# Optimization experiments

Measured on AMD Instinct MI355X. Metric: run time of the kernel, lower is better.

## Reference

```python
import jax, jax.numpy as jnp
import numpy as np

T, B, A, I, H, L = 256, 64, 512, 1024, 1024, 2
STDV = 1.0 / np.sqrt(H)

def _uniform(key, shape):
    return jax.random.uniform(key, shape, jnp.float32, -STDV, STDV)

def setup_inputs() -> dict:
    key = jax.random.key(0)
    ks = jax.random.split(key, 11)
    return {
        "attention": jax.random.normal(ks[0], (T, B, A), jnp.float32),
        "x": jax.random.normal(ks[1], (T, B, I), jnp.float32),
        "ping": jax.random.normal(ks[2], (B,), jnp.float32),  # unused by module
        "h0": jax.random.normal(ks[3], (L, B, H), jnp.float32),
        "c0": jax.random.normal(ks[4], (L, B, H), jnp.float32),
        "weight_ah": _uniform(ks[5], (L, A, 4 * H)),
        "weight_ih": _uniform(ks[6], (L, I, 4 * H)),  # input_size == hidden_size so layers stack
        "weight_hh": _uniform(ks[7], (L, H, 4 * H)),
        "bias_ah": _uniform(ks[8], (L, 4 * H)),
        "bias_ih": _uniform(ks[9], (L, 4 * H)),
        "bias_hh": _uniform(ks[10], (L, 4 * H)),
    }

def reference(attention, x, ping, h0, c0, weight_ah, weight_ih, weight_hh, bias_ah, bias_ih, bias_hh):
    # Faithful to SACILSTM.forward: only attention[0] is used (fixed across t),
    # ping is unused; per layer l, state is initialized from init_states[l].
    a0 = attention[0]  # [B, A]
    inputs = x  # [T, B, I]
    h_lasts, c_lasts = [], []
    for l in range(h0.shape[0]):
        w_hh = weight_hh[l]
        # Precompute the time-invariant + input-dependent part of the gates.
        const = a0 @ weight_ah[l] + bias_ah[l] + bias_ih[l] + bias_hh[l]  # [B, 4H]
        xg = jnp.einsum('tbi,ij->tbj', inputs, weight_ih[l]) + const  # [T, B, 4H]

        def step(carry, xg_t):
            h, c = carry
            gates = xg_t + h @ w_hh
            i_g, f_g, g_g, o_g = jnp.split(gates, 4, axis=-1)
            c = jax.nn.sigmoid(f_g) * c + jax.nn.sigmoid(i_g) * jnp.tanh(g_g)
            h = jax.nn.sigmoid(o_g) * jnp.tanh(c)
            return (h, c), h

        (h_T, c_T), hs = jax.lax.scan(step, (h0[l], c0[l]), xg)
        inputs = hs  # [T, B, H] feeds next layer
        h_lasts.append(h_T)
        c_lasts.append(c_T)
    # (self.h[:, -1], (self.h[-1], self.c[-1])) flattened
    return hs, jnp.stack(h_lasts), jnp.stack(c_lasts)
```

## Files before the change

kernel.cpp:

```cpp
#include <hip/hip_runtime.h>
#include <hip/hip_bf16.h>
#include <stdint.h>

#define TT 256
#define BB 64
#define AA 512
#define II 1024
#define HH 1024
#define LL 2
#define BH 65536
#define B4H 262144
#define OUT_HL 16777216
#define OUT_CL (16777216 + 131072)
#define NBLK 256

typedef __attribute__((ext_vector_type(8))) short bf16x8;
typedef __attribute__((ext_vector_type(4))) float f32x4;
typedef __attribute__((ext_vector_type(4))) unsigned int u32x4;
typedef __attribute__((ext_vector_type(2))) unsigned int u32x2;

__device__ __forceinline__ ushort f2bf(float v) {
    union { float f; uint32_t u; } x; x.f = v;
    uint32_t r = x.u + 0x7fff + ((x.u >> 16) & 1);
    return (ushort)(r >> 16);
}

__device__ __forceinline__ float sigf(float x) {
    return 1.f / (1.f + __expf(-x));
}


__global__ __launch_bounds__(256) void k_prep_wt(const float* __restrict__ wih,
                                                 const float* __restrict__ whh,
                                                 ushort* __restrict__ Wt) {
    __shared__ ushort tile[64][65];
    const int l = blockIdx.z;
    const int k0 = blockIdx.x * 64;
    const int col0 = blockIdx.y * 64;
    const int tid = threadIdx.x;
    const int cl = tid & 63, ks = tid >> 6;
    const float* src;
    int krow0;
    if (k0 < 1024) { src = wih + (size_t)l * 1024 * 4096; krow0 = k0; }
    else           { src = whh + (size_t)l * 1024 * 4096; krow0 = k0 - 1024; }
#pragma unroll
    for (int i = 0; i < 16; ++i) {
        int kl = ks + i * 4;
        tile[kl][cl] = f2bf(src[(size_t)(krow0 + kl) * 4096 + col0 + cl]);
    }
    __syncthreads();
    const int g0 = col0 >> 10, ub = col0 & 1023;
    ushort* dst = Wt + (size_t)l * 4096 * 2048;
    const int klane = tid & 63;
#pragma unroll
    for (int i = 0; i < 16; ++i) {
        int cl2 = (tid >> 6) + i * 4;
        int row = (ub + cl2) * 4 + g0;
        ushort* p = dst + (size_t)row * 2048 + k0 + klane;
        uint v = (uint)tile[klane][cl2];
        asm volatile("global_store_short %0, %1, off sc0 sc1"
                     :: "v"(p), "v"(v) : "memory");
    }
}

__global__ __launch_bounds__(256) void k_cast_x(const float* __restrict__ x,
                                                ushort* __restrict__ xbfF) {
    int i = blockIdx.x * 256 + threadIdx.x;
    int k8 = i & 127, b = (i >> 7) & 63, t = i >> 13;
    const float4* xs = (const float4*)(x + (((size_t)t * 64 + b) * 1024 + k8 * 8));
    float4 a = xs[0], c = xs[1];
    uint4 pk;
    pk.x = (uint)f2bf(a.x) | ((uint)f2bf(a.y) << 16);
    pk.y = (uint)f2bf(a.z) | ((uint)f2bf(a.w) << 16);
    pk.z = (uint)f2bf(c.x) | ((uint)f2bf(c.y) << 16);
    pk.w = (uint)f2bf(c.z) | ((uint)f2bf(c.w) << 16);
    size_t off = (size_t)t * 65536 + (size_t)(b >> 4) * 16384 +
                 (size_t)(k8 >> 2) * 512 + (size_t)(k8 & 3) * 128 + (size_t)(b & 15) * 8;
    *(uint4*)(xbfF + off) = pk;
}

__global__ __launch_bounds__(256) void k_const(const float* __restrict__ attn,
                                               const float* __restrict__ wah,
                                               const float* __restrict__ bah,
                                               const float* __restrict__ bih,
                                               const float* __restrict__ bhh,
                                               float* __restrict__ constg) {
    const int tid = threadIdx.x;
    const int col = blockIdx.x * 256 + tid;
    const int b0 = blockIdx.y * 8;
    const int l = blockIdx.z;
    const float* W = wah + (size_t)l * 512 * 4096;
    float acc[8] = {0.f, 0.f, 0.f, 0.f, 0.f, 0.f, 0.f, 0.f};
    for (int k = 0; k < 512; ++k) {
        float wv = W[(size_t)k * 4096 + col];
#pragma unroll
        for (int j = 0; j < 8; ++j) acc[j] += attn[(b0 + j) * 512 + k] * wv;
    }
    float bias = bah[l * 4096 + col] + bih[l * 4096 + col] + bhh[l * 4096 + col];
    float* cg = constg + (size_t)l * B4H;
#pragma unroll
    for (int j = 0; j < 8; ++j) cg[(size_t)(b0 + j) * 4096 + col] = acc[j] + bias;
}

__global__ __launch_bounds__(256) void k_init(const float* __restrict__ h0,
                                              ushort* __restrict__ hs0F,
                                              ushort* __restrict__ h1s0,
                                              unsigned* __restrict__ flags) {
    int i = blockIdx.x * 256 + threadIdx.x;
    if (i < 16384) {
        int k8 = i & 127, b = (i >> 7) & 63, l = i >> 13;
        const float* src = h0 + ((size_t)(l * 64 + b) * 1024 + k8 * 8);
        uint4 pk;
        pk.x = (uint)f2bf(src[0]) | ((uint)f2bf(src[1]) << 16);
        pk.y = (uint)f2bf(src[2]) | ((uint)f2bf(src[3]) << 16);
        pk.z = (uint)f2bf(src[4]) | ((uint)f2bf(src[5]) << 16);
        pk.w = (uint)f2bf(src[6]) | ((uint)f2bf(src[7]) << 16);
        size_t off = (size_t)(b >> 4) * 16384 + (size_t)(k8 >> 2) * 512 +
                     (size_t)(k8 & 3) * 128 + (size_t)(b & 15) * 8;
        *(uint4*)((l == 0 ? hs0F : h1s0) + off) = pk;
    }
    if (i < NBLK) flags[i] = 0u;
}

#define ISSUE(BUF, BASE)                                                       \
    do {                                                                       \
        _Pragma("unroll")                                                      \
        for (int _i = 0; _i < 8; ++_i)                                         \
            asm volatile("global_load_dwordx4 %0, %1, off"                     \
                         : "=v"(BUF[_i]) : "v"((BASE) + _i * 512));            \
    } while (0)

#define CONSUME2(BUF, c, N, A0, A1)                                            \
    do {                                                                       \
        asm volatile("s_waitcnt vmcnt(" #N ")" ::: "memory");                  \
        __builtin_amdgcn_sched_barrier(0x100);                                 \
        _Pragma("unroll")                                                      \
        for (int _i = 0; _i < 8; ++_i) {                                       \
            int _ktg = kh * 32 + (c) * 8 + _i;                                 \
            bf16x8 _b0 = *(const bf16x8*)(wlds + (size_t)_ktg * 1024 + lane * 8);       \
            bf16x8 _b1 = *(const bf16x8*)(wlds + (size_t)_ktg * 1024 + 512 + lane * 8); \
            A0 = __builtin_amdgcn_mfma_f32_16x16x32_bf16(BUF[_i], _b0, A0, 0, 0, 0);    \
            A1 = __builtin_amdgcn_mfma_f32_16x16x32_bf16(BUF[_i], _b1, A1, 0, 0, 0);    \
        }                                                                      \
    } while (0)

#define LOADCOMPUTE(AL)                                                        \
    do {                                                                       \
        const ushort* _a = (AL);                                               \
        ISSUE(bufA, _a + 0 * 4096);                                            \
        ISSUE(bufB, _a + 1 * 4096);                                            \
        ISSUE(bufC, _a + 2 * 4096);                                            \
        ISSUE(bufD, _a + 3 * 4096);                                            \
        CONSUME2(bufA, 0, 24, aE0, aE1);                                       \
        CONSUME2(bufB, 1, 16, aO0, aO1);                                       \
        CONSUME2(bufC, 2, 8,  aE0, aE1);                                       \
        CONSUME2(bufD, 3, 0,  aO0, aO1);                                       \
        const int _cc = lane & 15, _r0 = (lane >> 4) * 4;                      \
        _Pragma("unroll")                                                      \
        for (int _r = 0; _r < 4; ++_r) {                                       \
            gt[kh][m][0][_r0 + _r][_cc] = aE0[_r] + aO0[_r];                   \
            gt[kh][m][1][_r0 + _r][_cc] = aE1[_r] + aO1[_r];                   \
        }                                                                      \
    } while (0)

#define POLL128(FB, TGT)                                                       \
    do {                                                                       \
        const unsigned* _fp = (FB) + lane * 2;                                 \
        while (true) {                                                         \
            u32x2 _f;                                                          \
            asm volatile("global_load_dwordx2 %0, %1, off sc0 sc1\n\t"         \
                         "s_waitcnt vmcnt(0)"                                  \
                         : "=v"(_f) : "v"(_fp) : "memory");                    \
            if (__all(_f.x >= (TGT) && _f.y >= (TGT))) break;                  \
            __builtin_amdgcn_s_sleep(1);                                       \
        }                                                                      \
    } while (0)

__global__ __launch_bounds__(512, 2) void k_persist(
        const ushort* __restrict__ xbfF,
        ushort* __restrict__ hs0F,
        const ushort* __restrict__ h1s0,
        ushort* Wt,
        const float* __restrict__ constg,
        const float* __restrict__ c0,
        float* __restrict__ out,
        unsigned* __restrict__ flags) {
    __shared__ ushort wlds[65536];
    __shared__ float gt[2][4][2][16][18];

    const int tid = threadIdx.x;
    const int w = tid >> 6, lane = tid & 63;
    const int kh = w >> 2, m = w & 3;
    const int bid = blockIdx.x;
    const int layer = bid >> 7, ub = bid & 127;
    const int u0g = ub * 8;

    {
        bf16x8 vst[16];
#pragma unroll
        for (int i = 0; i < 16; ++i) {
            int c = i * 512 + tid;
            int lp = c & 63, nt = (c >> 6) & 1, ktg = c >> 7;
            int colp = u0g * 4 + nt * 16 + (lp & 15);
            int kk = ktg * 32 + (lp >> 4) * 8;
            const ushort* src = Wt + ((size_t)(layer * 4096 + colp)) * 2048 + kk;
            asm volatile("global_load_dwordx4 %0, %1, off sc0 sc1"
                         : "=v"(vst[i]) : "v"(src));
        }
        asm volatile("s_waitcnt vmcnt(0)" ::: "memory");
        __builtin_amdgcn_sched_barrier(0);
#pragma unroll
        for (int i = 0; i < 16; ++i) {
            int c = i * 512 + tid;
            *(bf16x8*)(wlds + (size_t)c * 8) = vst[i];
        }
    }

    const int b_e = (w << 3) | (lane >> 3);
    const int u_off = lane & 7;
    const int u_e = u0g + u_off;
    float cg[4];
#pragma unroll
    for (int g = 0; g < 4; ++g)
        cg[g] = constg[(size_t)layer * B4H + (size_t)b_e * 4096 + g * 1024 + u_e];
    float creg = c0[layer * BH + b_e * 1024 + u_e];
    const int mb = b_e >> 4, blb = b_e & 15, ntb = u_off >> 2, cpb = (u_off & 3) * 4;
    const size_t hoffL = (size_t)(b_e >> 4) * 16384 + (size_t)(ub >> 2) * 512 +
                         (size_t)(ub & 3) * 128 + (size_t)(b_e & 15) * 8;

    const size_t fro = (size_t)m * 16384 + (size_t)lane * 8;

    __syncthreads();

    const int sBeg = layer ? 1 : 0;
    const int sEnd = layer ? TT : (TT - 1);
    for (int s = sBeg; s <= sEnd; ++s) {
        const int t1 = s - 1;
        bf16x8 bufA[8], bufB[8], bufC[8], bufD[8];
        f32x4 aE0 = {0.f,0.f,0.f,0.f}, aO0 = {0.f,0.f,0.f,0.f};
        f32x4 aE1 = {0.f,0.f,0.f,0.f}, aO1 = {0.f,0.f,0.f,0.f};

        if (layer == 0) {
            if (kh == 0) LOADCOMPUTE(xbfF + (size_t)s * 65536 + fro);
            if (s >= 1 && w == 0) POLL128(flags, (unsigned)s);
            __syncthreads();
            if (kh == 1) LOADCOMPUTE(hs0F + (size_t)s * 65536 + fro);
        } else {
            if (w == 0) POLL128(flags, (unsigned)s);
            __syncthreads();
            if (kh == 0 && w != 0)
                LOADCOMPUTE(hs0F + (size_t)s * 65536 + fro);
            if (w == 0 && s >= 2) POLL128(flags + 128, (unsigned)s);
            __syncthreads();
            if (kh == 1) {
                const ushort* Al = (t1 == 0 ? h1s0
                                   : (const ushort*)Wt + (size_t)(t1 - 1) * 65536) + fro;
                LOADCOMPUTE(Al);
            } else if (w == 0) {
                LOADCOMPUTE(hs0F + (size_t)s * 65536 + fro);
            }
        }
        __syncthreads();

        float g4[4];
#pragma unroll
        for (int g = 0; g < 4; ++g)
            g4[g] = gt[0][mb][ntb][blb][cpb + g] + gt[1][mb][ntb][blb][cpb + g] + cg[g];
        float si = sigf(g4[0]), sf = sigf(g4[1]), so = sigf(g4[3]);
        float cn = sf * creg + si * (2.f * sigf(2.f * g4[2]) - 1.f);
        float hv = so * (2.f * sigf(2.f * cn) - 1.f);
        creg = cn;
        uint hb = (uint)f2bf(hv);
        uint p0 = __shfl(hb, (lane & 56) + 0), p1 = __shfl(hb, (lane & 56) + 1);
        uint p2 = __shfl(hb, (lane & 56) + 2), p3 = __shfl(hb, (lane & 56) + 3);
        uint p4 = __shfl(hb, (lane & 56) + 4), p5 = __shfl(hb, (lane & 56) + 5);
        uint p6 = __shfl(hb, (lane & 56) + 6), p7 = __shfl(hb, (lane & 56) + 7);
        u32x4 hp;
        hp.x = (p0 & 0xffffu) | (p1 << 16);
        hp.y = (p2 & 0xffffu) | (p3 << 16);
        hp.z = (p4 & 0xffffu) | (p5 << 16);
        hp.w = (p6 & 0xffffu) | (p7 << 16);
        ushort* hdst = (layer ? Wt + (size_t)t1 * 65536
                              : hs0F + (size_t)(s + 1) * 65536) + hoffL;
        if (u_off == 0)
            asm volatile("global_store_dwordx4 %0, %1, off sc0 sc1"
                         :: "v"(hdst), "v"(hp) : "memory");

        asm volatile("s_waitcnt vmcnt(0)" ::: "memory");
        __syncthreads();
        if (tid == 0) {
            unsigned tgt = (unsigned)(s + 1);
            unsigned* fp = flags + layer * 128 + ub;
            asm volatile("global_store_dword %0, %1, off sc0 sc1"
                         :: "v"(fp), "v"(tgt) : "memory");
        }

        if (layer == 1) {
            float o0 = __shfl(hv, (lane & 56) + 0), o1 = __shfl(hv, (lane & 56) + 1);
            float o2 = __shfl(hv, (lane & 56) + 2), o3 = __shfl(hv, (lane & 56) + 3);
            float o4 = __shfl(hv, (lane & 56) + 4), o5 = __shfl(hv, (lane & 56) + 5);
            float o6 = __shfl(hv, (lane & 56) + 6), o7 = __shfl(hv, (lane & 56) + 7);
            if (u_off == 0) {
                float* op = out + (size_t)t1 * 65536 + (size_t)b_e * 1024 + u0g;
                float4 v0 = {o0, o1, o2, o3}, v1 = {o4, o5, o6, o7};
                *(float4*)op = v0;
                *(float4*)(op + 4) = v1;
            }
            if (t1 == TT - 1) {
                out[OUT_HL + BH + b_e * 1024 + u_e] = hv;
                out[OUT_CL + BH + b_e * 1024 + u_e] = cn;
            }
        } else if (s == TT - 1) {
            out[OUT_HL + b_e * 1024 + u_e] = hv;
            out[OUT_CL + b_e * 1024 + u_e] = cn;
        }
    }
}

extern "C" void kernel_launch(void* const* d_in, const int* in_sizes, int n_in,
                              void* d_out, int out_size, void* d_ws, size_t ws_size,
                              hipStream_t stream) {
    const float* attn = (const float*)d_in[0];
    const float* x    = (const float*)d_in[1];
    const float* h0   = (const float*)d_in[3];
    const float* c0   = (const float*)d_in[4];
    const float* wah  = (const float*)d_in[5];
    const float* wih  = (const float*)d_in[6];
    const float* whh  = (const float*)d_in[7];
    const float* bah  = (const float*)d_in[8];
    const float* bih  = (const float*)d_in[9];
    const float* bhh  = (const float*)d_in[10];
    float* out = (float*)d_out;

    char* ws = (char*)d_ws;
    ushort*   Wt     = (ushort*)(ws);
    ushort*   xbfF   = (ushort*)(ws + 33554432);
    ushort*   hs0F   = (ushort*)(ws + 67108864);
    ushort*   h1s0   = (ushort*)(ws + 100794368);
    float*    constg = (float*)(ws + 100925440);
    unsigned* flags  = (unsigned*)(ws + 103022592);

    hipLaunchKernelGGL(k_prep_wt, dim3(32, 64, 2), dim3(256), 0, stream, wih, whh, Wt);
    hipLaunchKernelGGL(k_cast_x, dim3(8192), dim3(256), 0, stream, x, xbfF);
    hipLaunchKernelGGL(k_const, dim3(16, 8, 2), dim3(256), 0, stream, attn, wah, bah, bih, bhh, constg);
    hipLaunchKernelGGL(k_init, dim3(64), dim3(256), 0, stream, h0, hs0F, h1s0, flags);

    void* args[] = { (void*)&xbfF, (void*)&hs0F, (void*)&h1s0, (void*)&Wt,
                     (void*)&constg, (void*)&c0, (void*)&out, (void*)&flags };
    hipLaunchCooperativeKernel((void*)k_persist, dim3(NBLK), dim3(512), args, 0, stream);
}
```

Measured before the change: 1.787 ms.

## Rebalance per-step K split across warp halves and merge layer-1 polls

In layer 0, both kh halves now split the x projection and the recurrent h projection evenly, each taking half of every K range, instead of one half doing x and the other doing h after the barrier. In layer 1, the two flag polls run concurrently on different warps before a single barrier, removing one __syncthreads per step and the serialized second poll. This shortens the critical path per timestep and balances MFMA work between warp groups. The trade-off is that layer 0 now does half the h-dependent load and compute after the poll on every warp, and in layer 1 the layer-0 input load waits for both flags.

```diff
diff --git a/kernel.cpp b/kernel.cpp
--- a/kernel.cpp
+++ b/kernel.cpp
@@ -130,36 +130,17 @@
                          : "=v"(BUF[_i]) : "v"((BASE) + _i * 512));            \
     } while (0)
 
-#define CONSUME2(BUF, c, N, A0, A1)                                            \
+#define CHUNK(BUF, KTG0, N, A0, A1)                                            \
     do {                                                                       \
         asm volatile("s_waitcnt vmcnt(" #N ")" ::: "memory");                  \
         __builtin_amdgcn_sched_barrier(0x100);                                 \
         _Pragma("unroll")                                                      \
         for (int _i = 0; _i < 8; ++_i) {                                       \
-            int _ktg = kh * 32 + (c) * 8 + _i;                                 \
+            int _ktg = (KTG0) + _i;                                            \
             bf16x8 _b0 = *(const bf16x8*)(wlds + (size_t)_ktg * 1024 + lane * 8);       \
             bf16x8 _b1 = *(const bf16x8*)(wlds + (size_t)_ktg * 1024 + 512 + lane * 8); \
             A0 = __builtin_amdgcn_mfma_f32_16x16x32_bf16(BUF[_i], _b0, A0, 0, 0, 0);    \
             A1 = __builtin_amdgcn_mfma_f32_16x16x32_bf16(BUF[_i], _b1, A1, 0, 0, 0);    \
-        }                                                                      \
-    } while (0)
-
-#define LOADCOMPUTE(AL)                                                        \
-    do {                                                                       \
-        const ushort* _a = (AL);                                               \
-        ISSUE(bufA, _a + 0 * 4096);                                            \
-        ISSUE(bufB, _a + 1 * 4096);                                            \
-        ISSUE(bufC, _a + 2 * 4096);                                            \
-        ISSUE(bufD, _a + 3 * 4096);                                            \
-        CONSUME2(bufA, 0, 24, aE0, aE1);                                       \
-        CONSUME2(bufB, 1, 16, aO0, aO1);                                       \
-        CONSUME2(bufC, 2, 8,  aE0, aE1);                                       \
-        CONSUME2(bufD, 3, 0,  aO0, aO1);                                       \
-        const int _cc = lane & 15, _r0 = (lane >> 4) * 4;                      \
-        _Pragma("unroll")                                                      \
-        for (int _r = 0; _r < 4; ++_r) {                                       \
-            gt[kh][m][0][_r0 + _r][_cc] = aE0[_r] + aO0[_r];                   \
-            gt[kh][m][1][_r0 + _r][_cc] = aE1[_r] + aO1[_r];                   \
         }                                                                      \
     } while (0)
 
@@ -225,8 +206,8 @@
         cg[g] = constg[(size_t)layer * B4H + (size_t)b_e * 4096 + g * 1024 + u_e];
     float creg = c0[layer * BH + b_e * 1024 + u_e];
     const int mb = b_e >> 4, blb = b_e & 15, ntb = u_off >> 2, cpb = (u_off & 3) * 4;
-    const size_t hoffL = (size_t)(b_e >> 4) * 16384 + (size_t)(ub >> 2) * 512 +
-                         (size_t)(ub & 3) * 128 + (size_t)(b_e & 15) * 8;
+    const size_t hoffL = (size_t)mb * 16384 + (size_t)(ub >> 2) * 512 +
+                         (size_t)(ub & 3) * 128 + (size_t)blb * 8;
 
     const size_t fro = (size_t)m * 16384 + (size_t)lane * 8;
 
@@ -241,23 +222,48 @@
         f32x4 aE1 = {0.f,0.f,0.f,0.f}, aO1 = {0.f,0.f,0.f,0.f};
 
         if (layer == 0) {
-            if (kh == 0) LOADCOMPUTE(xbfF + (size_t)s * 65536 + fro);
+            {
+                const ushort* ax = xbfF + (size_t)s * 65536 + fro + kh * 8192;
+                ISSUE(bufA, ax);
+                ISSUE(bufB, ax + 4096);
+                CHUNK(bufA, kh * 16,     8, aE0, aE1);
+                CHUNK(bufB, kh * 16 + 8, 0, aO0, aO1);
+            }
             if (s >= 1 && w == 0) POLL128(flags, (unsigned)s);
             __syncthreads();
-            if (kh == 1) LOADCOMPUTE(hs0F + (size_t)s * 65536 + fro);
+            {
+                const ushort* ah = hs0F + (size_t)s * 65536 + fro + kh * 8192;
+                ISSUE(bufA, ah);
+                ISSUE(bufB, ah + 4096);
+                CHUNK(bufA, 32 + kh * 16,     8, aE0, aE1);
+                CHUNK(bufB, 32 + kh * 16 + 8, 0, aO0, aO1);
+            }
         } else {
             if (w == 0) POLL128(flags, (unsigned)s);
+            if (w == 4 && s >= 2) POLL128(flags + 128, (unsigned)s);
             __syncthreads();
-            if (kh == 0 && w != 0)
-                LOADCOMPUTE(hs0F + (size_t)s * 65536 + fro);
-            if (w == 0 && s >= 2) POLL128(flags + 128, (unsigned)s);
-            __syncthreads();
-            if (kh == 1) {
-                const ushort* Al = (t1 == 0 ? h1s0
-                                   : (const ushort*)Wt + (size_t)(t1 - 1) * 65536) + fro;
-                LOADCOMPUTE(Al);
-            } else if (w == 0) {
-                LOADCOMPUTE(hs0F + (size_t)s * 65536 + fro);
+            {
+                const ushort* a = (kh == 0)
+                    ? hs0F + (size_t)s * 65536 + fro
+                    : (t1 == 0 ? h1s0 + fro
+                               : (const ushort*)Wt + (size_t)(t1 - 1) * 65536 + fro);
+                ISSUE(bufA, a);
+                ISSUE(bufB, a + 4096);
+                ISSUE(bufC, a + 8192);
+                ISSUE(bufD, a + 12288);
+                CHUNK(bufA, kh * 32,      24, aE0, aE1);
+                CHUNK(bufB, kh * 32 + 8,  16, aO0, aO1);
+                CHUNK(bufC, kh * 32 + 16,  8, aE0, aE1);
+                CHUNK(bufD, kh * 32 + 24,  0, aO0, aO1);
+            }
+        }
+
+        {
+            const int cc = lane & 15, r0 = (lane >> 4) * 4;
+#pragma unroll
+            for (int r = 0; r < 4; ++r) {
+                gt[kh][m][0][r0 + r][cc] = aE0[r] + aO0[r];
+                gt[kh][m][1][r0 + r][cc] = aE1[r] + aO1[r];
             }
         }
         __syncthreads();
```

Result: faster. 1.681 ms (-5.9%).
